# Kernel optimization log

Hardware: AMD Instinct MI355X
Metric: run time of the kernel (lower is better)

Reference implementation:

```python
import jax, jax.numpy as jnp
import numpy as np

B = 128        # batch
N = 4096       # FLAGS.network_node
D_IN = 32      # embedding_in_size
D_OUT = 32     # embedding_out_size


def setup_inputs() -> dict:
    key = jax.random.key(0)
    k1, k2, k3, k4 = jax.random.split(key, 4)
    inputs = jax.random.normal(k1, (B, N * D_IN), dtype=jnp.float32)
    # mean-aggregation neighbor matrix: random nonneg, row-normalized (get_neibhour_nodes_matrix_mean)
    raw = jax.random.uniform(k2, (N, N), dtype=jnp.float32)
    adj = raw / jnp.sum(raw, axis=1, keepdims=True)
    # glorot uniform init as in source
    r = np.sqrt(6.0 / (D_IN + D_OUT)).astype(np.float32)
    W_neigh = jax.random.uniform(k3, (D_IN, D_OUT), minval=-r, maxval=r, dtype=jnp.float32)
    W_self = jax.random.uniform(k4, (D_IN, D_OUT), minval=-r, maxval=r, dtype=jnp.float32)
    return {"inputs": inputs, "adj": adj, "W_neigh": W_neigh, "W_self": W_self, "batch_train": 0}


def reference(inputs, adj, W_neigh, W_self, batch_train):
    # Math: relu(x @ (I_N (x) W_self + A (x) W_neigh))
    # Kronecker vec-trick: reshape x to [B, N, D_IN]; then
    #   x @ (A (x) W) reshaped = einsum('bip,ij,pq->bjq', x3, A, W)
    x3 = inputs.reshape(B, N, D_IN)
    self_part = jnp.einsum('bnp,pq->bnq', x3, W_self)            # I_N (x) W_self
    tmp = jnp.einsum('bip,pq->biq', x3, W_neigh)                  # apply small weight first
    neigh_part = jnp.einsum('biq,ij->bjq', tmp, adj)              # aggregate over graph
    out = jax.nn.relu(self_part + neigh_part)
    return out.reshape(B, N * D_OUT)
```

## Files before the change

### kernel.cpp

```cpp
#include <hip/hip_runtime.h>
#include <hip/hip_bf16.h>

#define N_NODES 4096
#define BATCH   128
#define DD      32

typedef float  f32x4  __attribute__((ext_vector_type(4)));
typedef __bf16 bf16x8 __attribute__((ext_vector_type(8)));
typedef int    i32x8  __attribute__((ext_vector_type(8)));

__device__ __forceinline__ void async_copy16(const void* g, void* l) {
    __builtin_amdgcn_global_load_lds(
        (const __attribute__((address_space(1))) unsigned int*)g,
        (__attribute__((address_space(3))) unsigned int*)l,
        16, 0, 0);
}

__device__ __forceinline__ unsigned pack_fp8x4(float a, float b, float c, float d) {
    int v = __builtin_amdgcn_cvt_pk_fp8_f32(a, b, 0, false);
    v     = __builtin_amdgcn_cvt_pk_fp8_f32(c, d, v, true);
    return (unsigned)v;
}

__global__ __launch_bounds__(256) void k_prep(
    const float* __restrict__ x, const float* __restrict__ Wn,
    const float* __restrict__ Ws, unsigned char* __restrict__ T8,
    float* __restrict__ out)
{
    const int lane = threadIdx.x & 63;
    const int gw   = (blockIdx.x * 256 + threadIdx.x) >> 6;
    const int m    = lane & 15;
    const int quad = lane >> 4;

    bf16x8 bn[2], bs[2];
#pragma unroll
    for (int h = 0; h < 2; ++h) {
        const int n = m + h * 16;
#pragma unroll
        for (int j = 0; j < 8; ++j) {
            const int k = quad * 8 + j;
            bn[h][j] = (__bf16)Wn[k * 32 + n];
            bs[h][j] = (__bf16)Ws[k * 32 + n];
        }
    }

    for (int t = gw; t < 32768; t += 8192) {
        const int row0 = t << 4;
        const int b    = row0 >> 12;
        const int i0   = row0 & 4095;

        const float4* xp = (const float4*)(x + (size_t)(row0 + m) * DD + quad * 8);
        const float4 x0 = xp[0], x1 = xp[1];
        bf16x8 a;
        a[0] = (__bf16)x0.x; a[1] = (__bf16)x0.y; a[2] = (__bf16)x0.z; a[3] = (__bf16)x0.w;
        a[4] = (__bf16)x1.x; a[5] = (__bf16)x1.y; a[6] = (__bf16)x1.z; a[7] = (__bf16)x1.w;

        const f32x4 z = {};
        const f32x4 cT0 = __builtin_amdgcn_mfma_f32_16x16x32_bf16(a, bn[0], z, 0, 0, 0);
        const f32x4 cT1 = __builtin_amdgcn_mfma_f32_16x16x32_bf16(a, bn[1], z, 0, 0, 0);
        const f32x4 cU0 = __builtin_amdgcn_mfma_f32_16x16x32_bf16(a, bs[0], z, 0, 0, 0);
        const f32x4 cU1 = __builtin_amdgcn_mfma_f32_16x16x32_bf16(a, bs[1], z, 0, 0, 0);

        *(unsigned*)&T8[((size_t)(b * 32 + m))      * N_NODES + i0 + quad * 4] =
            pack_fp8x4(cT0[0], cT0[1], cT0[2], cT0[3]);
        *(unsigned*)&T8[((size_t)(b * 32 + m + 16)) * N_NODES + i0 + quad * 4] =
            pack_fp8x4(cT1[0], cT1[1], cT1[2], cT1[3]);

        float* ub = out + (size_t)b * (N_NODES * DD) + (size_t)(i0 + quad * 4) * DD;
#pragma unroll
        for (int r = 0; r < 4; ++r) {
            ub[r * DD + m]      = cU0[r];
            ub[r * DD + m + 16] = cU1[r];
        }
    }
}

__global__ __launch_bounds__(256) void k_transpose_adj(
    const float* __restrict__ adj, unsigned char* __restrict__ adjT8)
{
    __shared__ float ts[64][65];
    const int tid = threadIdx.x;
    const int cx  = tid & 63;
    const int cy  = tid >> 6;
    const int i0  = blockIdx.y << 6;
    const int j0  = blockIdx.x << 6;
#pragma unroll
    for (int r = 0; r < 16; ++r) {
        const int row = cy * 16 + r;
        ts[row][cx] = adj[(size_t)(i0 + row) * N_NODES + j0 + cx];
    }
    __syncthreads();
    const int il = (tid & 7) * 8;
    const int jb = tid >> 3;
#pragma unroll
    for (int rr = 0; rr < 2; ++rr) {
        const int jl = jb + rr * 32;
        float v[8];
#pragma unroll
        for (int k = 0; k < 8; ++k) v[k] = ts[il + k][jl] * 4096.0f;
        uint2 p;
        p.x = pack_fp8x4(v[0], v[1], v[2], v[3]);
        p.y = pack_fp8x4(v[4], v[5], v[6], v[7]);
        *(uint2*)&adjT8[(size_t)(j0 + jl) * N_NODES + i0 + il] = p;
    }
}

__global__ __launch_bounds__(256) void k_gemm_neigh(
    const unsigned char* __restrict__ A8,
    const unsigned char* __restrict__ B8,
    float* __restrict__ out)
{
    __shared__ alignas(16) unsigned char As[128 * 128];
    __shared__ alignas(16) unsigned char Bs[128 * 128];

    const int tid   = threadIdx.x;
    const int lane  = tid & 63;
    const int wave  = tid >> 6;
    const int bm    = blockIdx.y << 7;
    const int bn    = blockIdx.x << 7;
    const int waveM = (wave >> 1) << 6;
    const int waveN = (wave & 1) << 6;
    const int lr    = lane & 15;
    const int lq    = lane >> 4;

    f32x4 acc[4][4] = {};

    const unsigned char* ga = A8 + (size_t)(bm + (tid >> 3)) * 4096 + (tid & 7) * 16;
    const unsigned char* gb = B8 + (size_t)(bn + (tid >> 3)) * 4096 + (tid & 7) * 16;
    char* la = (char*)As + tid * 16;
    char* lb = (char*)Bs + tid * 16;

    for (int k0 = 0; k0 < 4096; k0 += 128) {
#pragma unroll
        for (int n = 0; n < 4; ++n) {
            async_copy16(ga + (size_t)(n * 32) * 4096 + k0, la + n * 4096);
            async_copy16(gb + (size_t)(n * 32) * 4096 + k0, lb + n * 4096);
        }
        __syncthreads();

        i32x8 af[4], bfr[4];
#pragma unroll
        for (int t = 0; t < 4; ++t) {
            af[t]  = *(const i32x8*)&As[(waveM + t * 16 + lr) * 128 + lq * 32];
            bfr[t] = *(const i32x8*)&Bs[(waveN + t * 16 + lr) * 128 + lq * 32];
        }
#pragma unroll
        for (int tm = 0; tm < 4; ++tm)
#pragma unroll
            for (int tn = 0; tn < 4; ++tn)
                acc[tm][tn] = __builtin_amdgcn_mfma_scale_f32_16x16x128_f8f6f4(
                    af[tm], bfr[tn], acc[tm][tn],
                    0, 0,
                    0, 0x7F,
                    0, 0x73);
        __syncthreads();
    }

#pragma unroll
    for (int tm = 0; tm < 4; ++tm) {
        const int gm0 = bm + waveM + tm * 16 + lq * 4;
        const int b   = gm0 >> 5;
        const int q0  = gm0 & 31;
#pragma unroll
        for (int tn = 0; tn < 4; ++tn) {
            const int gj = bn + waveN + tn * 16 + lr;
            float* p = out + (size_t)b * (N_NODES * DD) + (size_t)gj * DD + q0;
            const float4 u = *(const float4*)p;
            float4 v;
            v.x = fmaxf(acc[tm][tn][0] + u.x, 0.0f);
            v.y = fmaxf(acc[tm][tn][1] + u.y, 0.0f);
            v.z = fmaxf(acc[tm][tn][2] + u.z, 0.0f);
            v.w = fmaxf(acc[tm][tn][3] + u.w, 0.0f);
            *(float4*)p = v;
        }
    }
}

extern "C" void kernel_launch(void* const* d_in, const int* in_sizes, int n_in,
                              void* d_out, int out_size, void* d_ws, size_t ws_size,
                              hipStream_t stream) {
    const float* x   = (const float*)d_in[0];
    const float* adj = (const float*)d_in[1];
    const float* Wn  = (const float*)d_in[2];
    const float* Ws  = (const float*)d_in[3];
    float* out = (float*)d_out;

    unsigned char* T8    = (unsigned char*)d_ws;
    unsigned char* adjT8 = T8 + (size_t)N_NODES * N_NODES;

    hipLaunchKernelGGL(k_prep, dim3(2048), dim3(256), 0, stream, x, Wn, Ws, T8, out);
    hipLaunchKernelGGL(k_transpose_adj, dim3(64, 64), dim3(256), 0, stream, adj, adjT8);
    hipLaunchKernelGGL(k_gemm_neigh, dim3(32, 32), dim3(256), 0, stream, T8, adjT8, out);
}
```

Before: 291.9 us.

## Merge prep and adjacency transpose kernels; XOR-swizzle GEMM LDS tiles

Fuses the x-projection prep kernel and the adjacency transpose/quantize kernel into one launch, using block-index ranges to pick the path. This removes one kernel launch and lets the two independent passes overlap on the GPU. In the FP8 GEMM, the global-to-LDS copy now writes 16-byte chunks at XOR-swizzled column positions, and fragment reads undo the swizzle with two 16-byte reads instead of one 32-byte read. The swizzle is meant to cut LDS bank conflicts, at the cost of extra index arithmetic and more LDS read instructions.

New measurement: 273.0 us. -6.5%, faster.

```diff
diff --git a/kernel.cpp b/kernel.cpp
--- a/kernel.cpp
+++ b/kernel.cpp
@@ -7,7 +7,11 @@
 
 typedef float  f32x4  __attribute__((ext_vector_type(4)));
 typedef __bf16 bf16x8 __attribute__((ext_vector_type(8)));
+typedef int    i32x4  __attribute__((ext_vector_type(4)));
 typedef int    i32x8  __attribute__((ext_vector_type(8)));
+
+#define PREP_BLOCKS 2048
+#define TR_BLOCKS   4096
 
 __device__ __forceinline__ void async_copy16(const void* g, void* l) {
     __builtin_amdgcn_global_load_lds(
@@ -22,86 +26,87 @@
     return (unsigned)v;
 }
 
-__global__ __launch_bounds__(256) void k_prep(
-    const float* __restrict__ x, const float* __restrict__ Wn,
-    const float* __restrict__ Ws, unsigned char* __restrict__ T8,
+__global__ __launch_bounds__(256) void k_pre(
+    const float* __restrict__ x, const float* __restrict__ adj,
+    const float* __restrict__ Wn, const float* __restrict__ Ws,
+    unsigned char* __restrict__ T8, unsigned char* __restrict__ adjT8,
     float* __restrict__ out)
-{
-    const int lane = threadIdx.x & 63;
-    const int gw   = (blockIdx.x * 256 + threadIdx.x) >> 6;
-    const int m    = lane & 15;
-    const int quad = lane >> 4;
-
-    bf16x8 bn[2], bs[2];
-#pragma unroll
-    for (int h = 0; h < 2; ++h) {
-        const int n = m + h * 16;
-#pragma unroll
-        for (int j = 0; j < 8; ++j) {
-            const int k = quad * 8 + j;
-            bn[h][j] = (__bf16)Wn[k * 32 + n];
-            bs[h][j] = (__bf16)Ws[k * 32 + n];
-        }
-    }
-
-    for (int t = gw; t < 32768; t += 8192) {
-        const int row0 = t << 4;
-        const int b    = row0 >> 12;
-        const int i0   = row0 & 4095;
-
-        const float4* xp = (const float4*)(x + (size_t)(row0 + m) * DD + quad * 8);
-        const float4 x0 = xp[0], x1 = xp[1];
-        bf16x8 a;
-        a[0] = (__bf16)x0.x; a[1] = (__bf16)x0.y; a[2] = (__bf16)x0.z; a[3] = (__bf16)x0.w;
-        a[4] = (__bf16)x1.x; a[5] = (__bf16)x1.y; a[6] = (__bf16)x1.z; a[7] = (__bf16)x1.w;
-
-        const f32x4 z = {};
-        const f32x4 cT0 = __builtin_amdgcn_mfma_f32_16x16x32_bf16(a, bn[0], z, 0, 0, 0);
-        const f32x4 cT1 = __builtin_amdgcn_mfma_f32_16x16x32_bf16(a, bn[1], z, 0, 0, 0);
-        const f32x4 cU0 = __builtin_amdgcn_mfma_f32_16x16x32_bf16(a, bs[0], z, 0, 0, 0);
-        const f32x4 cU1 = __builtin_amdgcn_mfma_f32_16x16x32_bf16(a, bs[1], z, 0, 0, 0);
-
-        *(unsigned*)&T8[((size_t)(b * 32 + m))      * N_NODES + i0 + quad * 4] =
-            pack_fp8x4(cT0[0], cT0[1], cT0[2], cT0[3]);
-        *(unsigned*)&T8[((size_t)(b * 32 + m + 16)) * N_NODES + i0 + quad * 4] =
-            pack_fp8x4(cT1[0], cT1[1], cT1[2], cT1[3]);
-
-        float* ub = out + (size_t)b * (N_NODES * DD) + (size_t)(i0 + quad * 4) * DD;
-#pragma unroll
-        for (int r = 0; r < 4; ++r) {
-            ub[r * DD + m]      = cU0[r];
-            ub[r * DD + m + 16] = cU1[r];
-        }
-    }
-}
-
-__global__ __launch_bounds__(256) void k_transpose_adj(
-    const float* __restrict__ adj, unsigned char* __restrict__ adjT8)
 {
     __shared__ float ts[64][65];
     const int tid = threadIdx.x;
-    const int cx  = tid & 63;
-    const int cy  = tid >> 6;
-    const int i0  = blockIdx.y << 6;
-    const int j0  = blockIdx.x << 6;
-#pragma unroll
-    for (int r = 0; r < 16; ++r) {
-        const int row = cy * 16 + r;
-        ts[row][cx] = adj[(size_t)(i0 + row) * N_NODES + j0 + cx];
-    }
-    __syncthreads();
-    const int il = (tid & 7) * 8;
-    const int jb = tid >> 3;
-#pragma unroll
-    for (int rr = 0; rr < 2; ++rr) {
-        const int jl = jb + rr * 32;
-        float v[8];
-#pragma unroll
-        for (int k = 0; k < 8; ++k) v[k] = ts[il + k][jl] * 4096.0f;
-        uint2 p;
-        p.x = pack_fp8x4(v[0], v[1], v[2], v[3]);
-        p.y = pack_fp8x4(v[4], v[5], v[6], v[7]);
-        *(uint2*)&adjT8[(size_t)(j0 + jl) * N_NODES + i0 + il] = p;
+
+    if (blockIdx.x < PREP_BLOCKS) {
+        const int lane = tid & 63;
+        const int gw   = (blockIdx.x * 256 + tid) >> 6;
+        const int m    = lane & 15;
+        const int quad = lane >> 4;
+
+        bf16x8 bn[2], bs[2];
+#pragma unroll
+        for (int h = 0; h < 2; ++h) {
+            const int n = m + h * 16;
+#pragma unroll
+            for (int j = 0; j < 8; ++j) {
+                const int k = quad * 8 + j;
+                bn[h][j] = (__bf16)Wn[k * 32 + n];
+                bs[h][j] = (__bf16)Ws[k * 32 + n];
+            }
+        }
+
+        for (int t = gw; t < 32768; t += 8192) {
+            const int row0 = t << 4;
+            const int b    = row0 >> 12;
+            const int i0   = row0 & 4095;
+
+            const float4* xp = (const float4*)(x + (size_t)(row0 + m) * DD + quad * 8);
+            const float4 x0 = xp[0], x1 = xp[1];
+            bf16x8 a;
+            a[0] = (__bf16)x0.x; a[1] = (__bf16)x0.y; a[2] = (__bf16)x0.z; a[3] = (__bf16)x0.w;
+            a[4] = (__bf16)x1.x; a[5] = (__bf16)x1.y; a[6] = (__bf16)x1.z; a[7] = (__bf16)x1.w;
+
+            const f32x4 z = {};
+            const f32x4 cT0 = __builtin_amdgcn_mfma_f32_16x16x32_bf16(a, bn[0], z, 0, 0, 0);
+            const f32x4 cT1 = __builtin_amdgcn_mfma_f32_16x16x32_bf16(a, bn[1], z, 0, 0, 0);
+            const f32x4 cU0 = __builtin_amdgcn_mfma_f32_16x16x32_bf16(a, bs[0], z, 0, 0, 0);
+            const f32x4 cU1 = __builtin_amdgcn_mfma_f32_16x16x32_bf16(a, bs[1], z, 0, 0, 0);
+
+            *(unsigned*)&T8[((size_t)(b * 32 + m))      * N_NODES + i0 + quad * 4] =
+                pack_fp8x4(cT0[0], cT0[1], cT0[2], cT0[3]);
+            *(unsigned*)&T8[((size_t)(b * 32 + m + 16)) * N_NODES + i0 + quad * 4] =
+                pack_fp8x4(cT1[0], cT1[1], cT1[2], cT1[3]);
+
+            float* ub = out + (size_t)b * (N_NODES * DD) + (size_t)(i0 + quad * 4) * DD;
+#pragma unroll
+            for (int r = 0; r < 4; ++r) {
+                ub[r * DD + m]      = cU0[r];
+                ub[r * DD + m + 16] = cU1[r];
+            }
+        }
+    } else {
+        const int bid = blockIdx.x - PREP_BLOCKS;
+        const int cx  = tid & 63;
+        const int cy  = tid >> 6;
+        const int i0  = (bid >> 6) << 6;
+        const int j0  = (bid & 63) << 6;
+#pragma unroll
+        for (int r = 0; r < 16; ++r) {
+            const int row = cy * 16 + r;
+            ts[row][cx] = adj[(size_t)(i0 + row) * N_NODES + j0 + cx];
+        }
+        __syncthreads();
+        const int il = (tid & 7) * 8;
+        const int jb = tid >> 3;
+#pragma unroll
+        for (int rr = 0; rr < 2; ++rr) {
+            const int jl = jb + rr * 32;
+            float v[8];
+#pragma unroll
+            for (int k = 0; k < 8; ++k) v[k] = ts[il + k][jl] * 4096.0f;
+            uint2 p;
+            p.x = pack_fp8x4(v[0], v[1], v[2], v[3]);
+            p.y = pack_fp8x4(v[4], v[5], v[6], v[7]);
+            *(uint2*)&adjT8[(size_t)(j0 + jl) * N_NODES + i0 + il] = p;
+        }
     }
 }
 
@@ -122,11 +127,14 @@
     const int waveN = (wave & 1) << 6;
     const int lr    = lane & 15;
     const int lq    = lane >> 4;
+    const int sw    = lr & 7;
 
     f32x4 acc[4][4] = {};
 
-    const unsigned char* ga = A8 + (size_t)(bm + (tid >> 3)) * 4096 + (tid & 7) * 16;
-    const unsigned char* gb = B8 + (size_t)(bn + (tid >> 3)) * 4096 + (tid & 7) * 16;
+    const int srow = tid >> 3;
+    const int scol = ((tid & 7) ^ (srow & 7)) * 16;
+    const unsigned char* ga = A8 + (size_t)(bm + srow) * 4096 + scol;
+    const unsigned char* gb = B8 + (size_t)(bn + srow) * 4096 + scol;
     char* la = (char*)As + tid * 16;
     char* lb = (char*)Bs + tid * 16;
 
@@ -141,8 +149,18 @@
         i32x8 af[4], bfr[4];
 #pragma unroll
         for (int t = 0; t < 4; ++t) {
-            af[t]  = *(const i32x8*)&As[(waveM + t * 16 + lr) * 128 + lq * 32];
-            bfr[t] = *(const i32x8*)&Bs[(waveN + t * 16 + lr) * 128 + lq * 32];
+            const int ra = (waveM + t * 16 + lr) * 128;
+            const int rb = (waveN + t * 16 + lr) * 128;
+            const int c0 = ((2 * lq)     ^ sw) * 16;
+            const int c1 = ((2 * lq + 1) ^ sw) * 16;
+            const i32x4 alo = *(const i32x4*)&As[ra + c0];
+            const i32x4 ahi = *(const i32x4*)&As[ra + c1];
+            const i32x4 blo = *(const i32x4*)&Bs[rb + c0];
+            const i32x4 bhi = *(const i32x4*)&Bs[rb + c1];
+            af[t][0]=alo[0]; af[t][1]=alo[1]; af[t][2]=alo[2]; af[t][3]=alo[3];
+            af[t][4]=ahi[0]; af[t][5]=ahi[1]; af[t][6]=ahi[2]; af[t][7]=ahi[3];
+            bfr[t][0]=blo[0]; bfr[t][1]=blo[1]; bfr[t][2]=blo[2]; bfr[t][3]=blo[3];
+            bfr[t][4]=bhi[0]; bfr[t][5]=bhi[1]; bfr[t][6]=bhi[2]; bfr[t][7]=bhi[3];
         }
 #pragma unroll
         for (int tm = 0; tm < 4; ++tm)
@@ -188,7 +206,7 @@
     unsigned char* T8    = (unsigned char*)d_ws;
     unsigned char* adjT8 = T8 + (size_t)N_NODES * N_NODES;
 
-    hipLaunchKernelGGL(k_prep, dim3(2048), dim3(256), 0, stream, x, Wn, Ws, T8, out);
-    hipLaunchKernelGGL(k_transpose_adj, dim3(64, 64), dim3(256), 0, stream, adj, adjT8);
+    hipLaunchKernelGGL(k_pre, dim3(PREP_BLOCKS + TR_BLOCKS), dim3(256), 0, stream,
+                       x, adj, Wn, Ws, T8, adjT8, out);
     hipLaunchKernelGGL(k_gemm_neigh, dim3(32, 32), dim3(256), 0, stream, T8, adjT8, out);
 }
```
